# Performance work log

Hardware: AMD Instinct MI355X
Metric: run time of the kernel (lower is better)

The kernel has to match this reference:

```python
import jax, jax.numpy as jnp
import numpy as np


def _knn_idx(pts, k):
    # pts: [N, d] -> indices of k nearest neighbors (incl. self, loop=True) [N, k]
    sq = jnp.sum(pts * pts, axis=-1)
    d2 = sq[:, None] + sq[None, :] - 2.0 * (pts @ pts.T)  # [N, N] squared dists
    _, idx = jax.lax.top_k(-d2, k)  # k smallest distances
    return idx


def _graph_conv(x, nbr, Wr, br, Ws):
    # x: [B, N, d_in], nbr: [B, N, k]. GraphConv (aggr='add'):
    # out_i = W_rel @ sum_j x_j + b_rel + W_root @ x_i
    gathered = jax.vmap(lambda xb, ib: xb[ib])(x, nbr)  # [B, N, k, d_in]
    agg = gathered.sum(axis=2)                          # [B, N, d_in]
    return agg @ Wr.T + br + x @ Ws.T


def setup_inputs() -> dict:
    key = jax.random.key(0)
    ks = jax.random.split(key, 10)
    B, N, D, H = 16, 2048, 3, 128
    s = lambda fi, fo: (2.0 / (fi + fo)) ** 0.5
    return {
        "point_cloud": jax.random.normal(ks[0], (B, N, D), dtype=jnp.float32),
        "W1r": jax.random.normal(ks[1], (H, D), dtype=jnp.float32) * s(D, H),
        "b1": jnp.zeros((H,), dtype=jnp.float32),
        "W1s": jax.random.normal(ks[2], (H, D), dtype=jnp.float32) * s(D, H),
        "W2r": jax.random.normal(ks[3], (H, H), dtype=jnp.float32) * s(H, H),
        "b2": jnp.zeros((H,), dtype=jnp.float32),
        "W2s": jax.random.normal(ks[4], (H, H), dtype=jnp.float32) * s(H, H),
        "W3r": jax.random.normal(ks[5], (H, H), dtype=jnp.float32) * s(H, H),
        "b3": jnp.zeros((H,), dtype=jnp.float32),
        "W3s": jax.random.normal(ks[6], (H, H), dtype=jnp.float32) * s(H, H),
        "k": 16,
    }


def reference(point_cloud, W1r, b1, W1s, W2r, b2, W2s, W3r, b3, W3s, k):
    # knn graph per batch element (loop=True: self-loop included, d(i,i)=0)
    nbr = jax.vmap(lambda p: _knn_idx(p, k))(point_cloud)  # [B, N, k]
    x = jax.nn.relu(_graph_conv(point_cloud, nbr, W1r, b1, W1s))
    x = jax.nn.relu(_graph_conv(x, nbr, W2r, b2, W2s))
    x = _graph_conv(x, nbr, W3r, b3, W3s)
    return x  # [B, N, output_dim]
```

## Files before the change

kernel.cpp:

```cpp
#include <hip/hip_runtime.h>
#include <math.h>

#define NPTS 2048
#define BATCH 16
#define KNN 16
#define HID 128
#define NPOINTS (BATCH * NPTS)
#define RPB 8
#define CAP 64
#define KNN_BLOCKS (NPOINTS / RPB)

typedef __attribute__((ext_vector_type(8))) short bf16x8;
typedef __attribute__((ext_vector_type(4))) float f32x4;

__device__ inline unsigned short f2bf(float f) {
    unsigned u = __float_as_uint(f);
    return (unsigned short)((u + 0x7FFFu + ((u >> 16) & 1u)) >> 16);
}
__device__ inline float bflo(unsigned v) { return __uint_as_float(v << 16); }
__device__ inline float bfhi(unsigned v) { return __uint_as_float(v & 0xFFFF0000u); }


__global__ __launch_bounds__(512) void knn_kernel(
    const float* __restrict__ pc, int* __restrict__ nbr,
    const float* __restrict__ W1r, const float* __restrict__ b1,
    const float* __restrict__ W1s, unsigned short* __restrict__ x1T,
    const float* __restrict__ W2r, const float* __restrict__ W2s,
    const float* __restrict__ W3r, const float* __restrict__ W3s,
    unsigned short* __restrict__ wT)
{
    __shared__ __align__(16) float4 pts[NPTS];
    __shared__ unsigned ckey[RPB][CAP];
    __shared__ unsigned cidx[RPB][CAP];
    __shared__ __align__(16) unsigned short xst[RPB][HID];

    if (blockIdx.x >= KNN_BLOCKS) {
        int g = (blockIdx.x - KNN_BLOCKS) * 2048 + (int)threadIdx.x * 4;
        #pragma unroll
        for (int u = 0; u < 4; ++u) {
            int g2 = g + u;
            int mm = g2 >> 14;
            int e = g2 & 16383;
            int r = e >> 7, cch = e & 127;
            const float* s = (mm == 0) ? W2r : (mm == 1) ? W2s
                           : (mm == 2) ? W3r : W3s;
            wT[mm * 16384 + ((cch >> 3) * 128 + r) * 8 + (cch & 7)] = f2bf(s[e]);
        }
        return;
    }

    const int b = blockIdx.x >> 8;
    const int rblk = blockIdx.x & 255;
    const float* p = pc + (size_t)b * NPTS * 3;

    for (int t = threadIdx.x; t < NPTS; t += 512) {
        float x = p[t * 3 + 0], y = p[t * 3 + 1], z = p[t * 3 + 2];
        pts[t] = make_float4(x, y, z, x * x + y * y + z * z);
    }
    __syncthreads();

    const int w = threadIdx.x >> 6;
    const int lane = threadIdx.x & 63;
    const int i = rblk * RPB + w;
    const float4 pi = pts[i];
    const float piw16 = pi.w + 16.0f;

    unsigned key[32];
    unsigned km = 0xFFFFFFFFu;
    #pragma unroll
    for (int t = 0; t < 32; ++t) {
        float4 c = pts[t * 64 + lane];
        float dot = fmaf(pi.x, c.x, fmaf(pi.y, c.y, pi.z * c.z));
        float d2 = fmaf(-2.0f, dot, piw16 + c.w);
        key[t] = __float_as_uint(d2);
        km = min(km, key[t]);
    }

    unsigned v = km;
    #pragma unroll
    for (int k = 2; k <= 64; k <<= 1) {
        #pragma unroll
        for (int j = k >> 1; j > 0; j >>= 1) {
            unsigned o = (unsigned)__shfl_xor((int)v, j, 64);
            bool sel = ((lane & k) == 0) == ((lane & j) == 0);
            v = sel ? min(v, o) : max(v, o);
        }
    }
    const unsigned T0 = (unsigned)__shfl((int)v, 15, 64);

    unsigned base = 0;
    #pragma unroll 1
    for (int t = 0; t < 32; ++t) {
        bool pred = key[t] <= T0;
        unsigned long long mask = __ballot(pred);
        if (mask) {
            unsigned prefix = __builtin_amdgcn_mbcnt_hi(
                (unsigned)(mask >> 32),
                __builtin_amdgcn_mbcnt_lo((unsigned)mask, 0));
            unsigned pos = base + prefix;
            if (pred && pos < CAP) {
                ckey[w][pos] = key[t];
                cidx[w][pos] = (unsigned)(t * 64 + lane);
            }
            base += (unsigned)__popcll(mask);
        }
    }
    __threadfence_block();
    const int m = (int)base;

    int* out = nbr + ((size_t)b * NPTS + i) * KNN;
    float ax = 0.f, ay = 0.f, az = 0.f;

    if (m <= CAP) {
        unsigned k0 = (lane < m) ? ckey[w][lane] : 0xFFFFFFFFu;
        int r0 = 0;
        #pragma unroll 2
        for (int jj = 0; jj < m; ++jj) {
            unsigned kj = ckey[w][jj];
            r0 += (kj < k0) || (kj == k0 && jj < lane);
        }
        if (lane < m && r0 < KNN) {
            unsigned j = cidx[w][lane];
            out[r0] = (int)j;
            float4 q = pts[j]; ax += q.x; ay += q.y; az += q.z;
        }
    } else {
        unsigned T = 0;
        #pragma unroll 1
        for (int bit = 31; bit >= 0; --bit) {
            unsigned trial = T | (1u << bit);
            int cnt = 0;
            #pragma unroll
            for (int t = 0; t < 32; ++t) cnt += (key[t] < trial);
            #pragma unroll
            for (int off = 32; off; off >>= 1)
                cnt += __shfl_xor(cnt, off, 64);
            if (cnt < KNN) T = trial;
        }
        unsigned bs = 0;
        #pragma unroll 1
        for (int t = 0; t < 32; ++t) {
            bool p1 = key[t] < T;
            unsigned long long mask = __ballot(p1);
            if (mask) {
                unsigned prefix = __builtin_amdgcn_mbcnt_hi(
                    (unsigned)(mask >> 32),
                    __builtin_amdgcn_mbcnt_lo((unsigned)mask, 0));
                if (p1) {
                    out[bs + prefix] = t * 64 + lane;
                    float4 q = pts[t * 64 + lane];
                    ax += q.x; ay += q.y; az += q.z;
                }
                bs += (unsigned)__popcll(mask);
            }
        }
        #pragma unroll 1
        for (int t = 0; t < 32 && bs < KNN; ++t) {
            bool p2 = key[t] == T;
            unsigned long long mask = __ballot(p2);
            if (mask) {
                unsigned prefix = __builtin_amdgcn_mbcnt_hi(
                    (unsigned)(mask >> 32),
                    __builtin_amdgcn_mbcnt_lo((unsigned)mask, 0));
                unsigned pos = bs + prefix;
                if (p2 && pos < KNN) {
                    out[pos] = t * 64 + lane;
                    float4 q = pts[t * 64 + lane];
                    ax += q.x; ay += q.y; az += q.z;
                }
                bs += (unsigned)__popcll(mask);
            }
        }
    }

    #pragma unroll
    for (int off = 32; off; off >>= 1) {
        ax += __shfl_xor(ax, off, 64);
        ay += __shfl_xor(ay, off, 64);
        az += __shfl_xor(az, off, 64);
    }

    #pragma unroll
    for (int hh = 0; hh < 2; ++hh) {
        int h = lane + hh * 64;
        float acc = b1[h];
        acc += W1r[h * 3 + 0] * ax + W1r[h * 3 + 1] * ay + W1r[h * 3 + 2] * az;
        acc += W1s[h * 3 + 0] * pi.x + W1s[h * 3 + 1] * pi.y + W1s[h * 3 + 2] * pi.z;
        xst[w][h] = f2bf(fmaxf(acc, 0.f));
    }
    __syncthreads();
    if (threadIdx.x < RPB * 16) {
        int pt = threadIdx.x & 7, cc = threadIdx.x >> 3;
        uint4 vv = *(const uint4*)&xst[pt][cc * 8];
        *(uint4*)&x1T[((size_t)cc * NPOINTS + (size_t)b * NPTS + rblk * RPB + pt) * 8] = vv;
    }
}

template <bool RELU, bool OUT_CHUNKED>
__global__ __launch_bounds__(512) void fusedconv_kernel(
    const unsigned short* __restrict__ xT, const int* __restrict__ nbr,
    const unsigned short* __restrict__ wTr, const unsigned short* __restrict__ wTs,
    const float* __restrict__ bias, void* __restrict__ outv)
{
    __shared__ __align__(16) char smem[64 * 132 * 4];
    unsigned short (*agg)[64][8] = (unsigned short (*)[64][8])smem;
    unsigned short (*obf)[136] = (unsigned short (*)[136])smem;
    float (*of32)[132] = (float (*)[132])smem;

    const int p0 = blockIdx.x * 64;
    const int b = blockIdx.x >> 5;
    const unsigned short* xbase = xT + (size_t)b * NPTS * 8;

    #pragma unroll
    for (int r = 0; r < 2; ++r) {
        int task = r * 512 + (int)threadIdx.x;
        int pt = task & 63, cc = task >> 6;
        const int4* nr4 = (const int4*)(nbr + (size_t)(p0 + pt) * KNN);
        const unsigned short* xp = xbase + (size_t)cc * ((size_t)NPOINTS * 8);
        float s[8] = {0, 0, 0, 0, 0, 0, 0, 0};
        #pragma unroll
        for (int q = 0; q < 4; ++q) {
            int4 n = nr4[q];
            uint4 v0 = *(const uint4*)(xp + (size_t)n.x * 8);
            uint4 v1 = *(const uint4*)(xp + (size_t)n.y * 8);
            uint4 v2 = *(const uint4*)(xp + (size_t)n.z * 8);
            uint4 v3 = *(const uint4*)(xp + (size_t)n.w * 8);
            s[0] += bflo(v0.x) + bflo(v1.x) + bflo(v2.x) + bflo(v3.x);
            s[1] += bfhi(v0.x) + bfhi(v1.x) + bfhi(v2.x) + bfhi(v3.x);
            s[2] += bflo(v0.y) + bflo(v1.y) + bflo(v2.y) + bflo(v3.y);
            s[3] += bfhi(v0.y) + bfhi(v1.y) + bfhi(v2.y) + bfhi(v3.y);
            s[4] += bflo(v0.z) + bflo(v1.z) + bflo(v2.z) + bflo(v3.z);
            s[5] += bfhi(v0.z) + bfhi(v1.z) + bfhi(v2.z) + bfhi(v3.z);
            s[6] += bflo(v0.w) + bflo(v1.w) + bflo(v2.w) + bflo(v3.w);
            s[7] += bfhi(v0.w) + bfhi(v1.w) + bfhi(v2.w) + bfhi(v3.w);
        }
        uint4 ov;
        ov.x = (unsigned)f2bf(s[0]) | ((unsigned)f2bf(s[1]) << 16);
        ov.y = (unsigned)f2bf(s[2]) | ((unsigned)f2bf(s[3]) << 16);
        ov.z = (unsigned)f2bf(s[4]) | ((unsigned)f2bf(s[5]) << 16);
        ov.w = (unsigned)f2bf(s[6]) | ((unsigned)f2bf(s[7]) << 16);
        *(uint4*)agg[cc][pt] = ov;
    }
    __syncthreads();

    const int wv = threadIdx.x >> 6;
    const int lane = threadIdx.x & 63;
    const int ptw = (wv & 1) * 32;
    const int h0w = (wv >> 1) * 32;
    const int row = lane & 15;
    const int quad = lane >> 4;

    f32x4 acc[2][2];
    #pragma unroll
    for (int i = 0; i < 2; ++i)
        #pragma unroll
        for (int n = 0; n < 2; ++n) acc[i][n] = (f32x4){0, 0, 0, 0};

    #pragma unroll
    for (int kc = 0; kc < 4; ++kc) {
        const int pl = quad + 4 * kc;
        bf16x8 a0 = *(const bf16x8*)agg[pl][ptw + row];
        bf16x8 a1 = *(const bf16x8*)agg[pl][ptw + 16 + row];
        #pragma unroll
        for (int n = 0; n < 2; ++n) {
            bf16x8 bb = *(const bf16x8*)(wTr + ((size_t)pl * HID + h0w + n * 16 + row) * 8);
            acc[0][n] = __builtin_amdgcn_mfma_f32_16x16x32_bf16(a0, bb, acc[0][n], 0, 0, 0);
            acc[1][n] = __builtin_amdgcn_mfma_f32_16x16x32_bf16(a1, bb, acc[1][n], 0, 0, 0);
        }
    }
    #pragma unroll
    for (int kc = 0; kc < 4; ++kc) {
        const int pl = quad + 4 * kc;
        bf16x8 a0 = *(const bf16x8*)(xT + ((size_t)pl * NPOINTS + p0 + ptw + row) * 8);
        bf16x8 a1 = *(const bf16x8*)(xT + ((size_t)pl * NPOINTS + p0 + ptw + 16 + row) * 8);
        #pragma unroll
        for (int n = 0; n < 2; ++n) {
            bf16x8 bb = *(const bf16x8*)(wTs + ((size_t)pl * HID + h0w + n * 16 + row) * 8);
            acc[0][n] = __builtin_amdgcn_mfma_f32_16x16x32_bf16(a0, bb, acc[0][n], 0, 0, 0);
            acc[1][n] = __builtin_amdgcn_mfma_f32_16x16x32_bf16(a1, bb, acc[1][n], 0, 0, 0);
        }
    }
    __syncthreads();

    #pragma unroll
    for (int n = 0; n < 2; ++n) {
        float bh = bias[h0w + n * 16 + row];
        #pragma unroll
        for (int i = 0; i < 2; ++i) {
            #pragma unroll
            for (int r = 0; r < 4; ++r) {
                int pt = ptw + i * 16 + quad * 4 + r;
                int hh = h0w + n * 16 + row;
                float vv = acc[i][n][r] + bh;
                if (RELU) vv = fmaxf(vv, 0.f);
                if (OUT_CHUNKED) obf[pt][hh] = f2bf(vv);
                else             of32[pt][hh] = vv;
            }
        }
    }
    __syncthreads();

    if (OUT_CHUNKED) {
        unsigned short* o = (unsigned short*)outv;
        #pragma unroll
        for (int q = 0; q < 2; ++q) {
            int task = q * 512 + threadIdx.x;
            int pt = task & 63, cc = task >> 6;
            *(uint4*)(o + ((size_t)cc * NPOINTS + p0 + pt) * 8) =
                *(const uint4*)&obf[pt][cc * 8];
        }
    } else {
        float* o = (float*)outv;
        #pragma unroll
        for (int q = 0; q < 4; ++q) {
            int task = q * 512 + threadIdx.x;
            int rr = task >> 5, ch = task & 31;
            *(float4*)(o + (size_t)(p0 + rr) * HID + ch * 4) =
                *(const float4*)&of32[rr][ch * 4];
        }
    }
}

extern "C" void kernel_launch(void* const* d_in, const int* in_sizes, int n_in,
                              void* d_out, int out_size, void* d_ws, size_t ws_size,
                              hipStream_t stream)
{
    const float* pc  = (const float*)d_in[0];
    const float* W1r = (const float*)d_in[1];
    const float* b1  = (const float*)d_in[2];
    const float* W1s = (const float*)d_in[3];
    const float* W2r = (const float*)d_in[4];
    const float* b2  = (const float*)d_in[5];
    const float* W2s = (const float*)d_in[6];
    const float* W3r = (const float*)d_in[7];
    const float* b3  = (const float*)d_in[8];
    const float* W3s = (const float*)d_in[9];
    float* out = (float*)d_out;

    char* ws = (char*)d_ws;
    const size_t MB = 1024 * 1024;
    const size_t XSZ = (size_t)NPOINTS * HID * 2;
    int*            nbr  = (int*)ws;
    unsigned short* x1T  = (unsigned short*)(ws + 2 * MB);
    unsigned short* x2T  = (unsigned short*)(ws + 2 * MB + XSZ);
    unsigned short* wT   = (unsigned short*)(ws + 2 * MB + 2 * XSZ);
    unsigned short* w2rT = wT;
    unsigned short* w2sT = wT + 16384;
    unsigned short* w3rT = wT + 32768;
    unsigned short* w3sT = wT + 49152;

    knn_kernel<<<KNN_BLOCKS + 32, 512, 0, stream>>>(
        pc, nbr, W1r, b1, W1s, x1T, W2r, W2s, W3r, W3s, wT);

    fusedconv_kernel<true, true><<<NPOINTS / 64, 512, 0, stream>>>(
        x1T, nbr, w2rT, w2sT, b2, x2T);

    fusedconv_kernel<false, false><<<NPOINTS / 64, 512, 0, stream>>>(
        x2T, nbr, w3rT, w3sT, b3, out);
}
```

Baseline: 194.9 us.

## Store intermediate features row-major so neighbor gathers read contiguous rows

```diff
diff --git a/kernel.cpp b/kernel.cpp
--- a/kernel.cpp
+++ b/kernel.cpp
@@ -24,7 +24,7 @@
 __global__ __launch_bounds__(512) void knn_kernel(
     const float* __restrict__ pc, int* __restrict__ nbr,
     const float* __restrict__ W1r, const float* __restrict__ b1,
-    const float* __restrict__ W1s, unsigned short* __restrict__ x1T,
+    const float* __restrict__ W1s, unsigned short* __restrict__ x1,
     const float* __restrict__ W2r, const float* __restrict__ W2s,
     const float* __restrict__ W3r, const float* __restrict__ W3s,
     unsigned short* __restrict__ wT)
@@ -190,15 +190,15 @@
     }
     __syncthreads();
     if (threadIdx.x < RPB * 16) {
-        int pt = threadIdx.x & 7, cc = threadIdx.x >> 3;
+        int pt = threadIdx.x >> 4, cc = threadIdx.x & 15;
         uint4 vv = *(const uint4*)&xst[pt][cc * 8];
-        *(uint4*)&x1T[((size_t)cc * NPOINTS + (size_t)b * NPTS + rblk * RPB + pt) * 8] = vv;
+        *(uint4*)&x1[((size_t)b * NPTS + rblk * RPB + pt) * HID + cc * 8] = vv;
     }
 }
 
-template <bool RELU, bool OUT_CHUNKED>
+template <bool RELU, bool OUT_BF16>
 __global__ __launch_bounds__(512) void fusedconv_kernel(
-    const unsigned short* __restrict__ xT, const int* __restrict__ nbr,
+    const unsigned short* __restrict__ xR, const int* __restrict__ nbr,
     const unsigned short* __restrict__ wTr, const unsigned short* __restrict__ wTs,
     const float* __restrict__ bias, void* __restrict__ outv)
 {
@@ -209,37 +209,42 @@
 
     const int p0 = blockIdx.x * 64;
     const int b = blockIdx.x >> 5;
-    const unsigned short* xbase = xT + (size_t)b * NPTS * 8;
-
-    #pragma unroll
-    for (int r = 0; r < 2; ++r) {
-        int task = r * 512 + (int)threadIdx.x;
-        int pt = task & 63, cc = task >> 6;
+    const unsigned short* xb = xR + (size_t)b * NPTS * HID;
+
+    {
+        const int pt = threadIdx.x >> 3;
+        const int sub = threadIdx.x & 7;
         const int4* nr4 = (const int4*)(nbr + (size_t)(p0 + pt) * KNN);
-        const unsigned short* xp = xbase + (size_t)cc * ((size_t)NPOINTS * 8);
-        float s[8] = {0, 0, 0, 0, 0, 0, 0, 0};
-        #pragma unroll
-        for (int q = 0; q < 4; ++q) {
-            int4 n = nr4[q];
-            uint4 v0 = *(const uint4*)(xp + (size_t)n.x * 8);
-            uint4 v1 = *(const uint4*)(xp + (size_t)n.y * 8);
-            uint4 v2 = *(const uint4*)(xp + (size_t)n.z * 8);
-            uint4 v3 = *(const uint4*)(xp + (size_t)n.w * 8);
-            s[0] += bflo(v0.x) + bflo(v1.x) + bflo(v2.x) + bflo(v3.x);
-            s[1] += bfhi(v0.x) + bfhi(v1.x) + bfhi(v2.x) + bfhi(v3.x);
-            s[2] += bflo(v0.y) + bflo(v1.y) + bflo(v2.y) + bflo(v3.y);
-            s[3] += bfhi(v0.y) + bfhi(v1.y) + bfhi(v2.y) + bfhi(v3.y);
-            s[4] += bflo(v0.z) + bflo(v1.z) + bflo(v2.z) + bflo(v3.z);
-            s[5] += bfhi(v0.z) + bfhi(v1.z) + bfhi(v2.z) + bfhi(v3.z);
-            s[6] += bflo(v0.w) + bflo(v1.w) + bflo(v2.w) + bflo(v3.w);
-            s[7] += bfhi(v0.w) + bfhi(v1.w) + bfhi(v2.w) + bfhi(v3.w);
-        }
-        uint4 ov;
-        ov.x = (unsigned)f2bf(s[0]) | ((unsigned)f2bf(s[1]) << 16);
-        ov.y = (unsigned)f2bf(s[2]) | ((unsigned)f2bf(s[3]) << 16);
-        ov.z = (unsigned)f2bf(s[4]) | ((unsigned)f2bf(s[5]) << 16);
-        ov.w = (unsigned)f2bf(s[6]) | ((unsigned)f2bf(s[7]) << 16);
-        *(uint4*)agg[cc][pt] = ov;
+        int4 n0 = nr4[0], n1 = nr4[1], n2 = nr4[2], n3 = nr4[3];
+        int idx[16] = {n0.x, n0.y, n0.z, n0.w, n1.x, n1.y, n1.z, n1.w,
+                       n2.x, n2.y, n2.z, n2.w, n3.x, n3.y, n3.z, n3.w};
+        float s0[8] = {0, 0, 0, 0, 0, 0, 0, 0};
+        float s1[8] = {0, 0, 0, 0, 0, 0, 0, 0};
+        #pragma unroll
+        for (int t = 0; t < KNN; ++t) {
+            const unsigned short* rowp = xb + (size_t)idx[t] * HID + sub * 8;
+            uint4 va = *(const uint4*)rowp;
+            uint4 vb = *(const uint4*)(rowp + 64);
+            s0[0] += bflo(va.x); s0[1] += bfhi(va.x);
+            s0[2] += bflo(va.y); s0[3] += bfhi(va.y);
+            s0[4] += bflo(va.z); s0[5] += bfhi(va.z);
+            s0[6] += bflo(va.w); s0[7] += bfhi(va.w);
+            s1[0] += bflo(vb.x); s1[1] += bfhi(vb.x);
+            s1[2] += bflo(vb.y); s1[3] += bfhi(vb.y);
+            s1[4] += bflo(vb.z); s1[5] += bfhi(vb.z);
+            s1[6] += bflo(vb.w); s1[7] += bfhi(vb.w);
+        }
+        uint4 o0, o1;
+        o0.x = (unsigned)f2bf(s0[0]) | ((unsigned)f2bf(s0[1]) << 16);
+        o0.y = (unsigned)f2bf(s0[2]) | ((unsigned)f2bf(s0[3]) << 16);
+        o0.z = (unsigned)f2bf(s0[4]) | ((unsigned)f2bf(s0[5]) << 16);
+        o0.w = (unsigned)f2bf(s0[6]) | ((unsigned)f2bf(s0[7]) << 16);
+        o1.x = (unsigned)f2bf(s1[0]) | ((unsigned)f2bf(s1[1]) << 16);
+        o1.y = (unsigned)f2bf(s1[2]) | ((unsigned)f2bf(s1[3]) << 16);
+        o1.z = (unsigned)f2bf(s1[4]) | ((unsigned)f2bf(s1[5]) << 16);
+        o1.w = (unsigned)f2bf(s1[6]) | ((unsigned)f2bf(s1[7]) << 16);
+        *(uint4*)agg[sub][pt] = o0;
+        *(uint4*)agg[sub + 8][pt] = o1;
     }
     __syncthreads();
 
@@ -271,8 +276,8 @@
     #pragma unroll
     for (int kc = 0; kc < 4; ++kc) {
         const int pl = quad + 4 * kc;
-        bf16x8 a0 = *(const bf16x8*)(xT + ((size_t)pl * NPOINTS + p0 + ptw + row) * 8);
-        bf16x8 a1 = *(const bf16x8*)(xT + ((size_t)pl * NPOINTS + p0 + ptw + 16 + row) * 8);
+        bf16x8 a0 = *(const bf16x8*)(xR + (size_t)(p0 + ptw + row) * HID + pl * 8);
+        bf16x8 a1 = *(const bf16x8*)(xR + (size_t)(p0 + ptw + 16 + row) * HID + pl * 8);
         #pragma unroll
         for (int n = 0; n < 2; ++n) {
             bf16x8 bb = *(const bf16x8*)(wTs + ((size_t)pl * HID + h0w + n * 16 + row) * 8);
@@ -293,20 +298,20 @@
                 int hh = h0w + n * 16 + row;
                 float vv = acc[i][n][r] + bh;
                 if (RELU) vv = fmaxf(vv, 0.f);
-                if (OUT_CHUNKED) obf[pt][hh] = f2bf(vv);
-                else             of32[pt][hh] = vv;
+                if (OUT_BF16) obf[pt][hh] = f2bf(vv);
+                else          of32[pt][hh] = vv;
             }
         }
     }
     __syncthreads();
 
-    if (OUT_CHUNKED) {
+    if (OUT_BF16) {
         unsigned short* o = (unsigned short*)outv;
         #pragma unroll
         for (int q = 0; q < 2; ++q) {
             int task = q * 512 + threadIdx.x;
-            int pt = task & 63, cc = task >> 6;
-            *(uint4*)(o + ((size_t)cc * NPOINTS + p0 + pt) * 8) =
+            int pt = task >> 4, cc = task & 15;
+            *(uint4*)(o + (size_t)(p0 + pt) * HID + cc * 8) =
                 *(const uint4*)&obf[pt][cc * 8];
         }
     } else {
@@ -341,8 +346,8 @@
     const size_t MB = 1024 * 1024;
     const size_t XSZ = (size_t)NPOINTS * HID * 2;
     int*            nbr  = (int*)ws;
-    unsigned short* x1T  = (unsigned short*)(ws + 2 * MB);
-    unsigned short* x2T  = (unsigned short*)(ws + 2 * MB + XSZ);
+    unsigned short* x1   = (unsigned short*)(ws + 2 * MB);
+    unsigned short* x2   = (unsigned short*)(ws + 2 * MB + XSZ);
     unsigned short* wT   = (unsigned short*)(ws + 2 * MB + 2 * XSZ);
     unsigned short* w2rT = wT;
     unsigned short* w2sT = wT + 16384;
@@ -350,11 +355,11 @@
     unsigned short* w3sT = wT + 49152;
 
     knn_kernel<<<KNN_BLOCKS + 32, 512, 0, stream>>>(
-        pc, nbr, W1r, b1, W1s, x1T, W2r, W2s, W3r, W3s, wT);
+        pc, nbr, W1r, b1, W1s, x1, W2r, W2s, W3r, W3s, wT);
 
     fusedconv_kernel<true, true><<<NPOINTS / 64, 512, 0, stream>>>(
-        x1T, nbr, w2rT, w2sT, b2, x2T);
+        x1, nbr, w2rT, w2sT, b2, x2);
 
     fusedconv_kernel<false, false><<<NPOINTS / 64, 512, 0, stream>>>(
-        x2T, nbr, w3rT, w3sT, b3, out);
+        x2, nbr, w3rT, w3sT, b3, out);
 }
```

New measurement: 166.1 us. 14.8% less time.
